# Kernel tuning notes

Measured on AMD Instinct MI355X. Metric: run time of the kernel, lower is better.

Reference implementation:

```python
import jax, jax.numpy as jnp
import numpy as np

B, T, F = 512, 256, 64
H = [128, 256, 128, 64]

def _glorot(key, shape):
    fan_in, fan_out = shape[0], shape[1]
    lim = np.sqrt(6.0 / (fan_in + fan_out))
    return jax.random.uniform(key, shape, jnp.float32, -lim, lim)

def setup_inputs() -> dict:
    key = jax.random.key(0)
    ks = jax.random.split(key, 16)
    inp = {"x": jax.random.normal(ks[0], (B, T, F), jnp.float32)}
    dims = [F] + H
    for i in range(4):
        inp[f"Wx{i+1}"] = _glorot(ks[1 + 3 * i], (dims[i], dims[i + 1]))
        # keras uses orthogonal recurrent init; scaled normal is an acceptable stand-in
        q, _ = jnp.linalg.qr(jax.random.normal(ks[2 + 3 * i], (dims[i + 1], dims[i + 1])))
        inp[f"Wh{i+1}"] = q.astype(jnp.float32)
        inp[f"b{i+1}"] = jnp.zeros((dims[i + 1],), jnp.float32)
    inp["Wd"] = _glorot(ks[13], (T * H[-1], 1))
    inp["bd"] = jnp.zeros((1,), jnp.float32)
    return inp

def simple_rnn(x, Wx, Wh, b):
    # x: [B, T, Fin] -> hidden sequence [B, T, H]; h_t = relu(x_t Wx + h_{t-1} Wh + b)
    xp = jnp.einsum('btf,fh->tbh', x, Wx) + b  # precompute input projection, time-major
    h0 = jnp.zeros((x.shape[0], Wh.shape[0]), x.dtype)
    def step(h, xt):
        h = jax.nn.relu(xt + h @ Wh)
        return h, h
    _, hs = jax.lax.scan(step, h0, xp)  # hs: [T, B, H]
    return jnp.transpose(hs, (1, 0, 2))

def reference(x, Wx1, Wh1, b1, Wx2, Wh2, b2, Wx3, Wh3, b3, Wx4, Wh4, b4, Wd, bd):
    h = simple_rnn(x, Wx1, Wh1, b1)   # dropout layers are identity at inference
    h = simple_rnn(h, Wx2, Wh2, b2)
    h = simple_rnn(h, Wx3, Wh3, b3)
    h = simple_rnn(h, Wx4, Wh4, b4)
    flat = h.reshape(h.shape[0], -1)  # [B, T*64]
    return flat @ Wd + bd             # [B, 1]
```

## Files before the change

kernel.cpp:

```cpp
#include <hip/hip_runtime.h>
#include <hip/hip_bf16.h>

#define BB 512
#define TT 256

typedef __attribute__((ext_vector_type(8))) short bf16x8;
typedef __attribute__((ext_vector_type(4))) float f32x4;

__device__ __forceinline__ unsigned short f2b(float f) {
    union { float f; unsigned u; } v; v.f = f;
    unsigned r = v.u + 0x7FFFu + ((v.u >> 16) & 1u);
    return (unsigned short)(r >> 16);
}
__device__ __forceinline__ float b2f(unsigned short h) {
    union { unsigned u; float f; } v; v.u = ((unsigned)h) << 16;
    return v.f;
}
__device__ __forceinline__ ushort2 pk2(float a, float b) {
    __hip_bfloat162 h = __float22bfloat162_rn(float2{a, b});
    union { __hip_bfloat162 h; ushort2 u; } v; v.h = h; return v.u;
}


__global__ __launch_bounds__(256) void cvt_tile4(const float* __restrict__ x,
                                                 unsigned short* __restrict__ xb,
                                                 const float* __restrict__ bd,
                                                 float* __restrict__ out) {
    if (blockIdx.x == 0) {
        out[threadIdx.x] = bd[0];
        out[threadIdx.x + 256] = bd[0];
    }
    const int s = blockIdx.x >> 6;
    const int tg = blockIdx.x & 63;
    const int wv = threadIdx.x >> 6;
    const int lane = threadIdx.x & 63;
    const int t = tg * 4 + wv;
    const int f0 = (lane & 15) * 4;
    const float* xt = x + ((size_t)s * 16 * TT + t) * 64;
    unsigned short* ob = xb + ((size_t)s * TT + t) * 1024;
#pragma unroll
    for (int it = 0; it < 4; ++it) {
        const int b = it * 4 + (lane >> 4);
        float4 v = *reinterpret_cast<const float4*>(xt + (size_t)b * (TT * 64) + f0);
        ushort2 lo = pk2(v.x, v.y), hi = pk2(v.z, v.w);
        ushort4 o; o.x = lo.x; o.y = lo.y; o.z = hi.x; o.w = hi.y;
        *reinterpret_cast<ushort4*>(ob + (f0 >> 3) * 128 + b * 8 + (f0 & 7)) = o;
    }
}

__global__ __launch_bounds__(512) __attribute__((amdgpu_waves_per_eu(2, 2))) void rnn4(
    const unsigned short* __restrict__ Xb,
    const float* __restrict__ Wx1, const float* __restrict__ Wh1, const float* __restrict__ b1,
    const float* __restrict__ Wx2, const float* __restrict__ Wh2, const float* __restrict__ b2,
    const float* __restrict__ Wx3, const float* __restrict__ Wh3, const float* __restrict__ b3,
    const float* __restrict__ Wx4, const float* __restrict__ Wh4, const float* __restrict__ b4,
    unsigned short* __restrict__ H4) {
    const int tid = threadIdx.x;
    const int s = blockIdx.x;
    const int w = tid >> 6;
    const int lane = tid & 63;
    const int l15 = lane & 15;
    const int quad = lane >> 4;
    const int rdo = quad * 128 + l15 * 8;

    __shared__ __align__(16) unsigned short hall[2][9216];

    bf16x8 wreg[48];
    f32x4 bvv[6];

#define LOADW(BASE, WP, H_, CB, KC_, MT_)                                          \
    _Pragma("unroll")                                                              \
    for (int mt = 0; mt < MT_; ++mt) {                                             \
        int m = (CB) + mt * 16 + l15;                                              \
        _Pragma("unroll")                                                          \
        for (int kc = 0; kc < KC_; ++kc)                                           \
            _Pragma("unroll")                                                      \
            for (int j = 0; j < 8; ++j)                                            \
                wreg[(BASE) + kc * MT_ + mt][j] =                                  \
                    (short)f2b(WP[(kc * 32 + quad * 8 + j) * H_ + m]);             \
    }
#define LOADBF(OFF, BP, CB, MT_)                                                   \
    _Pragma("unroll")                                                              \
    for (int mt = 0; mt < MT_; ++mt) {                                             \
        float4 t4v = *reinterpret_cast<const float4*>((BP) + (CB) + mt * 16 + quad * 4); \
        bvv[(OFF) + mt][0] = t4v.x; bvv[(OFF) + mt][1] = t4v.y;                    \
        bvv[(OFF) + mt][2] = t4v.z; bvv[(OFF) + mt][3] = t4v.w;                    \
    }

    if (w < 2) {
        LOADW(0,  Wh1, 128, w * 64, 4, 4)
        LOADW(16, Wx1, 128, w * 64, 2, 4)
        LOADW(24, Wh4, 64,  w * 32, 2, 2)
        LOADW(28, Wx4, 64,  w * 32, 4, 2)
        LOADBF(0, b1, w * 64, 4)
        LOADBF(4, b4, w * 32, 2)
    } else if (w < 6) {
        __builtin_amdgcn_s_setprio(1);
        LOADW(0,  Wh2, 256, (w - 2) * 64, 8, 4)
        LOADW(32, Wx2, 256, (w - 2) * 64, 4, 4)
        LOADBF(0, b2, (w - 2) * 64, 4)
    } else {
        LOADW(0,  Wh3, 128, (w - 6) * 64, 4, 4)
        LOADW(16, Wx3, 128, (w - 6) * 64, 8, 4)
        LOADBF(0, b3, (w - 6) * 64, 4)
    }
#undef LOADW
#undef LOADBF

    for (int i = tid; i < 2 * 9216; i += 512) (&hall[0][0])[i] = 0;

    const unsigned short* Xs = Xb + (size_t)s * TT * 1024;
    unsigned short* H4s = H4 + (size_t)s * TT * 1024;

    if (w < 2) {
#pragma unroll
        for (int kx = 0; kx < 2; ++kx) {
            wreg[36 + kx] = *reinterpret_cast<const bf16x8*>(&Xs[kx * 512 + rdo]);
            wreg[38 + kx] = *reinterpret_cast<const bf16x8*>(&Xs[1024 + kx * 512 + rdo]);
        }
    }
    __syncthreads();

    const unsigned short* xp0 = Xs + 2 * 1024 + rdo;
    const unsigned short* xp1 = Xs + 3 * 1024 + rdo;

    const int wro1 = (w * 8 + (quad >> 1)) * 128 + l15 * 8 + (quad & 1) * 4;
    const int wro4 = 8192 + (w * 4 + (quad >> 1)) * 128 + l15 * 8 + (quad & 1) * 4;
    const int wro2 = 2048 + ((w - 2) * 8 + (quad >> 1)) * 128 + l15 * 8 + (quad & 1) * 4;
    const int wro3 = 6144 + ((w - 6) * 8 + (quad >> 1)) * 128 + l15 * 8 + (quad & 1) * 4;

    unsigned short* op_e = H4s + 1024 + (wro4 - 8192);
    unsigned short* op_o = H4s + (wro4 - 8192);

#define PACKMK(ACC_MT)                                                             \
    ushort2 lo = pk2(fmaxf((ACC_MT)[0], 0.f), fmaxf((ACC_MT)[1], 0.f));            \
    ushort2 hi = pk2(fmaxf((ACC_MT)[2], 0.f), fmaxf((ACC_MT)[3], 0.f));            \
    ushort4 o; o.x = lo.x; o.y = lo.y; o.z = hi.x; o.w = hi.y;

#define STEP(TAU_, RP_, WP_, XAB, XPP, OPP)                                        \
    {                                                                              \
        const int tau_ = (TAU_);                                                   \
        const unsigned short* RB = &hall[RP_][0];                                  \
        unsigned short* WB = &hall[WP_][0];                                        \
        if (w < 2) {                                                               \
            if ((unsigned)tau_ < TT) {                                     \
                f32x4 acc[4];                                                      \
                _Pragma("unroll")                                                  \
                for (int mt = 0; mt < 4; ++mt)                                     \
                    acc[mt] = __builtin_amdgcn_mfma_f32_16x16x32_bf16(             \
                        wreg[16 + mt], wreg[(XAB) + 0], bvv[mt], 0, 0, 0);         \
                _Pragma("unroll")                                                  \
                for (int mt = 0; mt < 4; ++mt)                                     \
                    acc[mt] = __builtin_amdgcn_mfma_f32_16x16x32_bf16(             \
                        wreg[20 + mt], wreg[(XAB) + 1], acc[mt], 0, 0, 0);         \
                if (tau_ + 2 < TT) {                                               \
                    wreg[(XAB) + 0] = *reinterpret_cast<const bf16x8*>(XPP);       \
                    wreg[(XAB) + 1] = *reinterpret_cast<const bf16x8*>(XPP + 512); \
                    XPP += 2048;                                                   \
                }                                                                  \
                _Pragma("unroll")                                                  \
                for (int kc = 0; kc < 4; ++kc) {                                   \
                    bf16x8 af = *reinterpret_cast<const bf16x8*>(&RB[rdo + kc * 512]); \
                    _Pragma("unroll")                                              \
                    for (int mt = 0; mt < 4; ++mt)                                 \
                        acc[mt] = __builtin_amdgcn_mfma_f32_16x16x32_bf16(         \
                            wreg[kc * 4 + mt], af, acc[mt], 0, 0, 0);              \
                }                                                                  \
                _Pragma("unroll")                                                  \
                for (int mt = 0; mt < 4; ++mt) {                                   \
                    PACKMK(acc[mt])                                                \
                    *reinterpret_cast<ushort4*>(&WB[wro1 + mt * 256]) = o;         \
                }                                                                  \
            }                                                                      \
            if ((unsigned)(tau_ - 3) < TT) {                               \
                f32x4 acc[2];                                                      \
                {                                                                  \
                    bf16x8 af0 = *reinterpret_cast<const bf16x8*>(&RB[6144 + rdo]); \
                    _Pragma("unroll")                                              \
                    for (int mt = 0; mt < 2; ++mt)                                 \
                        acc[mt] = __builtin_amdgcn_mfma_f32_16x16x32_bf16(         \
                            wreg[28 + mt], af0, bvv[4 + mt], 0, 0, 0);             \
                }                                                                  \
                _Pragma("unroll")                                                  \
                for (int kx = 1; kx < 4; ++kx) {                                   \
                    bf16x8 af = *reinterpret_cast<const bf16x8*>(&RB[6144 + rdo + kx * 512]); \
                    _Pragma("unroll")                                              \
                    for (int mt = 0; mt < 2; ++mt)                                 \
                        acc[mt] = __builtin_amdgcn_mfma_f32_16x16x32_bf16(         \
                            wreg[28 + kx * 2 + mt], af, acc[mt], 0, 0, 0);         \
                }                                                                  \
                _Pragma("unroll")                                                  \
                for (int kc = 0; kc < 2; ++kc) {                                   \
                    bf16x8 af = *reinterpret_cast<const bf16x8*>(&RB[8192 + rdo + kc * 512]); \
                    _Pragma("unroll")                                              \
                    for (int mt = 0; mt < 2; ++mt)                                 \
                        acc[mt] = __builtin_amdgcn_mfma_f32_16x16x32_bf16(         \
                            wreg[24 + kc * 2 + mt], af, acc[mt], 0, 0, 0);         \
                }                                                                  \
                _Pragma("unroll")                                                  \
                for (int mt = 0; mt < 2; ++mt) {                                   \
                    PACKMK(acc[mt])                                                \
                    *reinterpret_cast<ushort4*>(&WB[wro4 + mt * 256]) = o;         \
                    *reinterpret_cast<ushort4*>(OPP + mt * 256) = o;               \
                }                                                                  \
                OPP += 2048;                                                       \
            }                                                                      \
        } else if (w < 6) {                                                        \
            if ((unsigned)(tau_ - 1) < TT) {                               \
                f32x4 acc[4];                                                      \
                {                                                                  \
                    bf16x8 af0 = *reinterpret_cast<const bf16x8*>(&RB[rdo]);       \
                    _Pragma("unroll")                                              \
                    for (int mt = 0; mt < 4; ++mt)                                 \
                        acc[mt] = __builtin_amdgcn_mfma_f32_16x16x32_bf16(         \
                            wreg[32 + mt], af0, bvv[mt], 0, 0, 0);                 \
                }                                                                  \
                _Pragma("unroll")                                                  \
                for (int kx = 1; kx < 4; ++kx) {                                   \
                    bf16x8 af = *reinterpret_cast<const bf16x8*>(&RB[rdo + kx * 512]); \
                    _Pragma("unroll")                                              \
                    for (int mt = 0; mt < 4; ++mt)                                 \
                        acc[mt] = __builtin_amdgcn_mfma_f32_16x16x32_bf16(         \
                            wreg[32 + kx * 4 + mt], af, acc[mt], 0, 0, 0);         \
                }                                                                  \
                _Pragma("unroll")                                                  \
                for (int kc = 0; kc < 8; ++kc) {                                   \
                    bf16x8 af = *reinterpret_cast<const bf16x8*>(&RB[2048 + rdo + kc * 512]); \
                    _Pragma("unroll")                                              \
                    for (int mt = 0; mt < 4; ++mt)                                 \
                        acc[mt] = __builtin_amdgcn_mfma_f32_16x16x32_bf16(         \
                            wreg[kc * 4 + mt], af, acc[mt], 0, 0, 0);              \
                }                                                                  \
                _Pragma("unroll")                                                  \
                for (int mt = 0; mt < 4; ++mt) {                                   \
                    PACKMK(acc[mt])                                                \
                    *reinterpret_cast<ushort4*>(&WB[wro2 + mt * 256]) = o;         \
                }                                                                  \
            }                                                                      \
        } else {                                                                   \
            if ((unsigned)(tau_ - 2) < TT) {                               \
                f32x4 acc[4];                                                      \
                {                                                                  \
                    bf16x8 af0 = *reinterpret_cast<const bf16x8*>(&RB[2048 + rdo]); \
                    _Pragma("unroll")                                              \
                    for (int mt = 0; mt < 4; ++mt)                                 \
                        acc[mt] = __builtin_amdgcn_mfma_f32_16x16x32_bf16(         \
                            wreg[16 + mt], af0, bvv[mt], 0, 0, 0);                 \
                }                                                                  \
                _Pragma("unroll")                                                  \
                for (int kx = 1; kx < 8; ++kx) {                                   \
                    bf16x8 af = *reinterpret_cast<const bf16x8*>(&RB[2048 + rdo + kx * 512]); \
                    _Pragma("unroll")                                              \
                    for (int mt = 0; mt < 4; ++mt)                                 \
                        acc[mt] = __builtin_amdgcn_mfma_f32_16x16x32_bf16(         \
                            wreg[16 + kx * 4 + mt], af, acc[mt], 0, 0, 0);         \
                }                                                                  \
                _Pragma("unroll")                                                  \
                for (int kc = 0; kc < 4; ++kc) {                                   \
                    bf16x8 af = *reinterpret_cast<const bf16x8*>(&RB[6144 + rdo + kc * 512]); \
                    _Pragma("unroll")                                              \
                    for (int mt = 0; mt < 4; ++mt)                                 \
                        acc[mt] = __builtin_amdgcn_mfma_f32_16x16x32_bf16(         \
                            wreg[kc * 4 + mt], af, acc[mt], 0, 0, 0);              \
                }                                                                  \
                _Pragma("unroll")                                                  \
                for (int mt = 0; mt < 4; ++mt) {                                   \
                    PACKMK(acc[mt])                                                \
                    *reinterpret_cast<ushort4*>(&WB[wro3 + mt * 256]) = o;         \
                }                                                                  \
            }                                                                      \
        }                                                                          \
        __builtin_amdgcn_s_waitcnt(0xC07F);                                        \
        __builtin_amdgcn_s_barrier();                                              \
    }

#pragma unroll 1
    for (int tau = 0; tau < TT + 3; tau += 2) {
        STEP(tau, 0, 1, 36, xp0, op_e)
        STEP(tau + 1, 1, 0, 38, xp1, op_o)
    }
#undef STEP
#undef PACKMK
}

__global__ __launch_bounds__(256) void dense_part(const unsigned short* __restrict__ Ht,
                                                  const float* __restrict__ Wd,
                                                  float* __restrict__ out) {
    __shared__ float red[16][17];
    const int s = blockIdx.x >> 3;
    const int tc = blockIdx.x & 7;
    const int tid = threadIdx.x;
    const int b = (tid >> 1) & 15;
    const int kbase = (tid >> 5) * 8 + (tid & 1) * 4;
    const unsigned short* base = Ht + ((size_t)s * TT + tc * 32) * 1024 + tid * 4;
    float acc = 0.f;
    for (int t = 0; t < 32; ++t) {
        ushort4 v = *reinterpret_cast<const ushort4*>(base + (size_t)t * 1024);
        const float* wd = &Wd[(tc * 32 + t) * 64 + kbase];
        acc += b2f(v.x) * wd[0] + b2f(v.y) * wd[1] + b2f(v.z) * wd[2] + b2f(v.w) * wd[3];
    }
    red[b][(tid >> 5) * 2 + (tid & 1)] = acc;
    __syncthreads();
    if (tid < 16) {
        float sum = 0.f;
#pragma unroll
        for (int j = 0; j < 16; ++j) sum += red[tid][j];
        atomicAdd(&out[s * 16 + tid], sum);
    }
}

extern "C" void kernel_launch(void* const* d_in, const int* in_sizes, int n_in,
                              void* d_out, int out_size, void* d_ws, size_t ws_size,
                              hipStream_t stream) {
    (void)in_sizes; (void)n_in; (void)out_size; (void)ws_size;
    const float* x   = (const float*)d_in[0];
    const float* Wx1 = (const float*)d_in[1];
    const float* Wh1 = (const float*)d_in[2];
    const float* b1  = (const float*)d_in[3];
    const float* Wx2 = (const float*)d_in[4];
    const float* Wh2 = (const float*)d_in[5];
    const float* b2  = (const float*)d_in[6];
    const float* Wx3 = (const float*)d_in[7];
    const float* Wh3 = (const float*)d_in[8];
    const float* b3  = (const float*)d_in[9];
    const float* Wx4 = (const float*)d_in[10];
    const float* Wh4 = (const float*)d_in[11];
    const float* b4  = (const float*)d_in[12];
    const float* Wd  = (const float*)d_in[13];
    const float* bd  = (const float*)d_in[14];
    float* out = (float*)d_out;

    char* ws = (char*)d_ws;
    unsigned short* xbT = (unsigned short*)(ws);
    unsigned short* H4  = (unsigned short*)(ws + 16777216);

    cvt_tile4<<<2048, 256, 0, stream>>>(x, xbT, bd, out);

    rnn4<<<32, 512, 0, stream>>>(xbT, Wx1, Wh1, b1, Wx2, Wh2, b2,
                                 Wx3, Wh3, b3, Wx4, Wh4, b4, H4);

    dense_part<<<256, 256, 0, stream>>>(H4, Wd, out);
}
```

Before: 421.7 us.

## Fuse dense head into RNN kernel and stage cvt transpose through LDS

The final dense projection moves into the tail of the recurrent kernel. Each block reads back its own H4 slice after a waitcnt and barrier, reduces it in LDS, adds the bias and writes the output directly. This removes a kernel launch and the atomics along with the separate out-initialisation. The input conversion kernel now loads rows with coalesced float4 reads into shared memory and writes 8-wide bf16 packs, where before it used strided per-lane accesses. Risks: the fused tail relies on H4s (not visible) and on global writes from the same block being visible after the barrier, and the dense work runs on only 32 blocks.

```diff
diff --git a/kernel.cpp b/kernel.cpp
--- a/kernel.cpp
+++ b/kernel.cpp
@@ -23,28 +23,35 @@
 
 
 __global__ __launch_bounds__(256) void cvt_tile4(const float* __restrict__ x,
-                                                 unsigned short* __restrict__ xb,
-                                                 const float* __restrict__ bd,
-                                                 float* __restrict__ out) {
-    if (blockIdx.x == 0) {
-        out[threadIdx.x] = bd[0];
-        out[threadIdx.x + 256] = bd[0];
-    }
+                                                 unsigned short* __restrict__ xb) {
+    __shared__ float xs[16][260];
     const int s = blockIdx.x >> 6;
     const int tg = blockIdx.x & 63;
-    const int wv = threadIdx.x >> 6;
-    const int lane = threadIdx.x & 63;
-    const int t = tg * 4 + wv;
-    const int f0 = (lane & 15) * 4;
-    const float* xt = x + ((size_t)s * 16 * TT + t) * 64;
-    unsigned short* ob = xb + ((size_t)s * TT + t) * 1024;
+    const int tid = threadIdx.x;
+    const float* xbase = x + ((size_t)(s * 16) * TT + tg * 4) * 64;
 #pragma unroll
     for (int it = 0; it < 4; ++it) {
-        const int b = it * 4 + (lane >> 4);
-        float4 v = *reinterpret_cast<const float4*>(xt + (size_t)b * (TT * 64) + f0);
-        ushort2 lo = pk2(v.x, v.y), hi = pk2(v.z, v.w);
-        ushort4 o; o.x = lo.x; o.y = lo.y; o.z = hi.x; o.w = hi.y;
-        *reinterpret_cast<ushort4*>(ob + (f0 >> 3) * 128 + b * 8 + (f0 & 7)) = o;
+        const int b = it * 4 + (tid >> 6);
+        const int r = tid & 63;
+        float4 v = *reinterpret_cast<const float4*>(xbase + (size_t)b * (TT * 64) + r * 4);
+        *reinterpret_cast<float4*>(&xs[b][r * 4]) = v;
+    }
+    __syncthreads();
+#pragma unroll
+    for (int it = 0; it < 2; ++it) {
+        const int t = it * 2 + (tid >> 7);
+        const int oct = (tid >> 4) & 7;
+        const int b = tid & 15;
+        const float* src = &xs[b][t * 64 + oct * 8];
+        float4 va = *reinterpret_cast<const float4*>(src);
+        float4 vb = *reinterpret_cast<const float4*>(src + 4);
+        ushort2 p0 = pk2(va.x, va.y), p1 = pk2(va.z, va.w);
+        ushort2 p2 = pk2(vb.x, vb.y), p3 = pk2(vb.z, vb.w);
+        ushort4 lo; lo.x = p0.x; lo.y = p0.y; lo.z = p1.x; lo.w = p1.y;
+        ushort4 hi; hi.x = p2.x; hi.y = p2.y; hi.z = p3.x; hi.w = p3.y;
+        unsigned short* ob = xb + ((size_t)(s * TT) + tg * 4 + t) * 1024 + oct * 128 + b * 8;
+        *reinterpret_cast<ushort4*>(ob) = lo;
+        *reinterpret_cast<ushort4*>(ob + 4) = hi;
     }
 }
 
@@ -54,7 +61,9 @@
     const float* __restrict__ Wx2, const float* __restrict__ Wh2, const float* __restrict__ b2,
     const float* __restrict__ Wx3, const float* __restrict__ Wh3, const float* __restrict__ b3,
     const float* __restrict__ Wx4, const float* __restrict__ Wh4, const float* __restrict__ b4,
-    unsigned short* __restrict__ H4) {
+    unsigned short* __restrict__ H4,
+    const float* __restrict__ Wd, const float* __restrict__ bd,
+    float* __restrict__ out) {
     const int tid = threadIdx.x;
     const int s = blockIdx.x;
     const int w = tid >> 6;
@@ -281,31 +290,41 @@
     }
 #undef STEP
 #undef PACKMK
-}
-
-__global__ __launch_bounds__(256) void dense_part(const unsigned short* __restrict__ Ht,
-                                                  const float* __restrict__ Wd,
-                                                  float* __restrict__ out) {
-    __shared__ float red[16][17];
-    const int s = blockIdx.x >> 3;
-    const int tc = blockIdx.x & 7;
-    const int tid = threadIdx.x;
-    const int b = (tid >> 1) & 15;
-    const int kbase = (tid >> 5) * 8 + (tid & 1) * 4;
-    const unsigned short* base = Ht + ((size_t)s * TT + tc * 32) * 1024 + tid * 4;
-    float acc = 0.f;
-    for (int t = 0; t < 32; ++t) {
-        ushort4 v = *reinterpret_cast<const ushort4*>(base + (size_t)t * 1024);
-        const float* wd = &Wd[(tc * 32 + t) * 64 + kbase];
-        acc += b2f(v.x) * wd[0] + b2f(v.y) * wd[1] + b2f(v.z) * wd[2] + b2f(v.w) * wd[3];
-    }
-    red[b][(tid >> 5) * 2 + (tid & 1)] = acc;
+
+    __builtin_amdgcn_s_waitcnt(0x0F70);
     __syncthreads();
-    if (tid < 16) {
-        float sum = 0.f;
+    {
+        float dacc = 0.f;
+        const unsigned short* gb = H4s + quad * 128 + l15 * 8;
+        const float* wb = Wd + quad * 8;
+#pragma unroll 4
+        for (int ti = 0; ti < 32; ++ti) {
+            const int t = w + ti * 8;
+            bf16x8 h0 = *reinterpret_cast<const bf16x8*>(gb + (size_t)t * 1024);
+            bf16x8 h1 = *reinterpret_cast<const bf16x8*>(gb + (size_t)t * 1024 + 512);
+            const float* wd = wb + t * 64;
+            float4 wa = *reinterpret_cast<const float4*>(wd);
+            float4 wc = *reinterpret_cast<const float4*>(wd + 4);
+            float4 we = *reinterpret_cast<const float4*>(wd + 32);
+            float4 wg = *reinterpret_cast<const float4*>(wd + 36);
+            dacc += b2f((unsigned short)h0[0]) * wa.x + b2f((unsigned short)h0[1]) * wa.y +
+                    b2f((unsigned short)h0[2]) * wa.z + b2f((unsigned short)h0[3]) * wa.w +
+                    b2f((unsigned short)h0[4]) * wc.x + b2f((unsigned short)h0[5]) * wc.y +
+                    b2f((unsigned short)h0[6]) * wc.z + b2f((unsigned short)h0[7]) * wc.w +
+                    b2f((unsigned short)h1[0]) * we.x + b2f((unsigned short)h1[1]) * we.y +
+                    b2f((unsigned short)h1[2]) * we.z + b2f((unsigned short)h1[3]) * we.w +
+                    b2f((unsigned short)h1[4]) * wg.x + b2f((unsigned short)h1[5]) * wg.y +
+                    b2f((unsigned short)h1[6]) * wg.z + b2f((unsigned short)h1[7]) * wg.w;
+        }
+        float* red = reinterpret_cast<float*>(&hall[0][0]);
+        red[(w * 4 + quad) * 16 + l15] = dacc;
+        __syncthreads();
+        if (tid < 16) {
+            float sum = bd[0];
 #pragma unroll
-        for (int j = 0; j < 16; ++j) sum += red[tid][j];
-        atomicAdd(&out[s * 16 + tid], sum);
+            for (int j = 0; j < 32; ++j) sum += red[j * 16 + tid];
+            out[s * 16 + tid] = sum;
+        }
     }
 }
 
@@ -334,10 +353,8 @@
     unsigned short* xbT = (unsigned short*)(ws);
     unsigned short* H4  = (unsigned short*)(ws + 16777216);
 
-    cvt_tile4<<<2048, 256, 0, stream>>>(x, xbT, bd, out);
+    cvt_tile4<<<2048, 256, 0, stream>>>(x, xbT);
 
     rnn4<<<32, 512, 0, stream>>>(xbT, Wx1, Wh1, b1, Wx2, Wh2, b2,
-                                 Wx3, Wh3, b3, Wx4, Wh4, b4, H4);
-
-    dense_part<<<256, 256, 0, stream>>>(H4, Wd, out);
-}
+                                 Wx3, Wh3, b3, Wx4, Wh4, b4, H4, Wd, bd, out);
+}
```

Result: no change. 423.5 us (+0.4%).

## Deepen layer wavefront pipeline with triple-buffered LDS and register prefetch

Applied to the files above, without the earlier changes.

The layered RNN wavefront moves from a two-buffer LDS ping-pong to a rotating three-buffer scheme, and each layer's stage skew grows from one step to two. Each wave group now loads the previous layer's input rows into registers (pf) one step ahead and does all LDS reads before issuing its MFMA chains, so LDS latency overlaps the previous barrier interval. The input conversion kernel is also rewritten to stage x through shared memory, giving coalesced reads and 16-byte writes. The cost is a longer pipeline fill and drain (TT+6 steps instead of TT+3), more LDS use and higher register pressure.

```diff
diff --git a/kernel.cpp b/kernel.cpp
--- a/kernel.cpp
+++ b/kernel.cpp
@@ -30,21 +30,34 @@
         out[threadIdx.x] = bd[0];
         out[threadIdx.x + 256] = bd[0];
     }
+    __shared__ float xs[16][260];
     const int s = blockIdx.x >> 6;
     const int tg = blockIdx.x & 63;
-    const int wv = threadIdx.x >> 6;
-    const int lane = threadIdx.x & 63;
-    const int t = tg * 4 + wv;
-    const int f0 = (lane & 15) * 4;
-    const float* xt = x + ((size_t)s * 16 * TT + t) * 64;
-    unsigned short* ob = xb + ((size_t)s * TT + t) * 1024;
+    const int tid = threadIdx.x;
+    const float* xbase = x + ((size_t)(s * 16) * TT + tg * 4) * 64;
 #pragma unroll
     for (int it = 0; it < 4; ++it) {
-        const int b = it * 4 + (lane >> 4);
-        float4 v = *reinterpret_cast<const float4*>(xt + (size_t)b * (TT * 64) + f0);
-        ushort2 lo = pk2(v.x, v.y), hi = pk2(v.z, v.w);
-        ushort4 o; o.x = lo.x; o.y = lo.y; o.z = hi.x; o.w = hi.y;
-        *reinterpret_cast<ushort4*>(ob + (f0 >> 3) * 128 + b * 8 + (f0 & 7)) = o;
+        const int b = it * 4 + (tid >> 6);
+        const int r = tid & 63;
+        float4 v = *reinterpret_cast<const float4*>(xbase + (size_t)b * (TT * 64) + r * 4);
+        *reinterpret_cast<float4*>(&xs[b][r * 4]) = v;
+    }
+    __syncthreads();
+#pragma unroll
+    for (int it = 0; it < 2; ++it) {
+        const int t = it * 2 + (tid >> 7);
+        const int oct = (tid >> 4) & 7;
+        const int b = tid & 15;
+        const float* src = &xs[b][t * 64 + oct * 8];
+        float4 va = *reinterpret_cast<const float4*>(src);
+        float4 vb = *reinterpret_cast<const float4*>(src + 4);
+        ushort2 p0 = pk2(va.x, va.y), p1 = pk2(va.z, va.w);
+        ushort2 p2 = pk2(vb.x, vb.y), p3 = pk2(vb.z, vb.w);
+        ushort4 lo; lo.x = p0.x; lo.y = p0.y; lo.z = p1.x; lo.w = p1.y;
+        ushort4 hi; hi.x = p2.x; hi.y = p2.y; hi.z = p3.x; hi.w = p3.y;
+        unsigned short* ob = xb + ((size_t)(s * TT) + tg * 4 + t) * 1024 + oct * 128 + b * 8;
+        *reinterpret_cast<ushort4*>(ob) = lo;
+        *reinterpret_cast<ushort4*>(ob + 4) = hi;
     }
 }
 
@@ -63,9 +76,10 @@
     const int quad = lane >> 4;
     const int rdo = quad * 128 + l15 * 8;
 
-    __shared__ __align__(16) unsigned short hall[2][9216];
+    __shared__ __align__(16) unsigned short hall[3][9216];
 
     bf16x8 wreg[48];
+    bf16x8 pf[4];
     f32x4 bvv[6];
 
 #define LOADW(BASE, WP, H_, CB, KC_, MT_)                                          \
@@ -107,7 +121,7 @@
 #undef LOADW
 #undef LOADBF
 
-    for (int i = tid; i < 2 * 9216; i += 512) (&hall[0][0])[i] = 0;
+    for (int i = tid; i < 3 * 9216; i += 512) (&hall[0][0])[i] = 0;
 
     const unsigned short* Xs = Xb + (size_t)s * TT * 1024;
     unsigned short* H4s = H4 + (size_t)s * TT * 1024;
@@ -129,21 +143,26 @@
     const int wro2 = 2048 + ((w - 2) * 8 + (quad >> 1)) * 128 + l15 * 8 + (quad & 1) * 4;
     const int wro3 = 6144 + ((w - 6) * 8 + (quad >> 1)) * 128 + l15 * 8 + (quad & 1) * 4;
 
-    unsigned short* op_e = H4s + 1024 + (wro4 - 8192);
-    unsigned short* op_o = H4s + (wro4 - 8192);
+    unsigned short* op_e = H4s + (wro4 - 8192);
+    unsigned short* op_o = H4s + 1024 + (wro4 - 8192);
 
 #define PACKMK(ACC_MT)                                                             \
     ushort2 lo = pk2(fmaxf((ACC_MT)[0], 0.f), fmaxf((ACC_MT)[1], 0.f));            \
     ushort2 hi = pk2(fmaxf((ACC_MT)[2], 0.f), fmaxf((ACC_MT)[3], 0.f));            \
     ushort4 o; o.x = lo.x; o.y = lo.y; o.z = hi.x; o.w = hi.y;
 
-#define STEP(TAU_, RP_, WP_, XAB, XPP, OPP)                                        \
+#define STEP(TAU_, RBP_, WBP_, IBP_, XAB, XPP, OPP)                                \
     {                                                                              \
         const int tau_ = (TAU_);                                                   \
-        const unsigned short* RB = &hall[RP_][0];                                  \
-        unsigned short* WB = &hall[WP_][0];                                        \
+        const unsigned short* RB = (RBP_);                                         \
+        unsigned short* WB = (WBP_);                                               \
+        const unsigned short* IB = (IBP_);                                         \
         if (w < 2) {                                                               \
-            if ((unsigned)tau_ < TT) {                                     \
+            if ((unsigned)tau_ < TT) {                            \
+                bf16x8 rf[4];                                                      \
+                _Pragma("unroll")                                                  \
+                for (int kc = 0; kc < 4; ++kc)                                     \
+                    rf[kc] = *reinterpret_cast<const bf16x8*>(&RB[rdo + kc * 512]); \
                 f32x4 acc[4];                                                      \
                 _Pragma("unroll")                                                  \
                 for (int mt = 0; mt < 4; ++mt)                                     \
@@ -159,44 +178,39 @@
                     XPP += 2048;                                                   \
                 }                                                                  \
                 _Pragma("unroll")                                                  \
-                for (int kc = 0; kc < 4; ++kc) {                                   \
-                    bf16x8 af = *reinterpret_cast<const bf16x8*>(&RB[rdo + kc * 512]); \
-                    _Pragma("unroll")                                              \
-                    for (int mt = 0; mt < 4; ++mt)                                 \
-                        acc[mt] = __builtin_amdgcn_mfma_f32_16x16x32_bf16(         \
-                            wreg[kc * 4 + mt], af, acc[mt], 0, 0, 0);              \
-                }                                                                  \
+                for (int kc = 0; kc < 4; ++kc)                                     \
+                    _Pragma("unroll")                                              \
+                    for (int mt = 0; mt < 4; ++mt)                                 \
+                        acc[mt] = __builtin_amdgcn_mfma_f32_16x16x32_bf16(         \
+                            wreg[kc * 4 + mt], rf[kc], acc[mt], 0, 0, 0);          \
                 _Pragma("unroll")                                                  \
                 for (int mt = 0; mt < 4; ++mt) {                                   \
                     PACKMK(acc[mt])                                                \
                     *reinterpret_cast<ushort4*>(&WB[wro1 + mt * 256]) = o;         \
                 }                                                                  \
             }                                                                      \
-            if ((unsigned)(tau_ - 3) < TT) {                               \
+            if ((unsigned)(tau_ - 6) < TT) {  \
+                bf16x8 rf4[2];                                                     \
+                _Pragma("unroll")                                                  \
+                for (int kc = 0; kc < 2; ++kc)                                     \
+                    rf4[kc] = *reinterpret_cast<const bf16x8*>(&RB[8192 + rdo + kc * 512]); \
                 f32x4 acc[2];                                                      \
-                {                                                                  \
-                    bf16x8 af0 = *reinterpret_cast<const bf16x8*>(&RB[6144 + rdo]); \
+                _Pragma("unroll")                                                  \
+                for (int mt = 0; mt < 2; ++mt)                                     \
+                    acc[mt] = __builtin_amdgcn_mfma_f32_16x16x32_bf16(             \
+                        wreg[28 + mt], pf[0], bvv[4 + mt], 0, 0, 0);               \
+                _Pragma("unroll")                                                  \
+                for (int kx = 1; kx < 4; ++kx)                                     \
                     _Pragma("unroll")                                              \
                     for (int mt = 0; mt < 2; ++mt)                                 \
                         acc[mt] = __builtin_amdgcn_mfma_f32_16x16x32_bf16(         \
-                            wreg[28 + mt], af0, bvv[4 + mt], 0, 0, 0);             \
-                }                                                                  \
-                _Pragma("unroll")                                                  \
-                for (int kx = 1; kx < 4; ++kx) {                                   \
-                    bf16x8 af = *reinterpret_cast<const bf16x8*>(&RB[6144 + rdo + kx * 512]); \
+                            wreg[28 + kx * 2 + mt], pf[kx], acc[mt], 0, 0, 0);     \
+                _Pragma("unroll")                                                  \
+                for (int kc = 0; kc < 2; ++kc)                                     \
                     _Pragma("unroll")                                              \
                     for (int mt = 0; mt < 2; ++mt)                                 \
                         acc[mt] = __builtin_amdgcn_mfma_f32_16x16x32_bf16(         \
-                            wreg[28 + kx * 2 + mt], af, acc[mt], 0, 0, 0);         \
-                }                                                                  \
-                _Pragma("unroll")                                                  \
-                for (int kc = 0; kc < 2; ++kc) {                                   \
-                    bf16x8 af = *reinterpret_cast<const bf16x8*>(&RB[8192 + rdo + kc * 512]); \
-                    _Pragma("unroll")                                              \
-                    for (int mt = 0; mt < 2; ++mt)                                 \
-                        acc[mt] = __builtin_amdgcn_mfma_f32_16x16x32_bf16(         \
-                            wreg[24 + kc * 2 + mt], af, acc[mt], 0, 0, 0);         \
-                }                                                                  \
+                            wreg[24 + kc * 2 + mt], rf4[kc], acc[mt], 0, 0, 0);    \
                 _Pragma("unroll")                                                  \
                 for (int mt = 0; mt < 2; ++mt) {                                   \
                     PACKMK(acc[mt])                                                \
@@ -205,79 +219,104 @@
                 }                                                                  \
                 OPP += 2048;                                                       \
             }                                                                      \
+            if ((unsigned)(tau_ - 5) < TT) {   \
+                _Pragma("unroll")                                                  \
+                for (int kx = 0; kx < 4; ++kx)                                     \
+                    pf[kx] = *reinterpret_cast<const bf16x8*>(&RB[6144 + rdo + kx * 512]); \
+            }                                                                      \
         } else if (w < 6) {                                                        \
-            if ((unsigned)(tau_ - 1) < TT) {                               \
+            if ((unsigned)(tau_ - 2) < TT) {  \
+                bf16x8 rf[8];                                                      \
+                _Pragma("unroll")                                                  \
+                for (int kc = 0; kc < 8; ++kc)                                     \
+                    rf[kc] = *reinterpret_cast<const bf16x8*>(&RB[2048 + rdo + kc * 512]); \
                 f32x4 acc[4];                                                      \
-                {                                                                  \
-                    bf16x8 af0 = *reinterpret_cast<const bf16x8*>(&RB[rdo]);       \
-                    _Pragma("unroll")                                              \
-                    for (int mt = 0; mt < 4; ++mt)                                 \
-                        acc[mt] = __builtin_amdgcn_mfma_f32_16x16x32_bf16(         \
-                            wreg[32 + mt], af0, bvv[mt], 0, 0, 0);                 \
-                }                                                                  \
-                _Pragma("unroll")                                                  \
-                for (int kx = 1; kx < 4; ++kx) {                                   \
-                    bf16x8 af = *reinterpret_cast<const bf16x8*>(&RB[rdo + kx * 512]); \
-                    _Pragma("unroll")                                              \
-                    for (int mt = 0; mt < 4; ++mt)                                 \
-                        acc[mt] = __builtin_amdgcn_mfma_f32_16x16x32_bf16(         \
-                            wreg[32 + kx * 4 + mt], af, acc[mt], 0, 0, 0);         \
-                }                                                                  \
-                _Pragma("unroll")                                                  \
-                for (int kc = 0; kc < 8; ++kc) {                                   \
-                    bf16x8 af = *reinterpret_cast<const bf16x8*>(&RB[2048 + rdo + kc * 512]); \
-                    _Pragma("unroll")                                              \
-                    for (int mt = 0; mt < 4; ++mt)                                 \
-                        acc[mt] = __builtin_amdgcn_mfma_f32_16x16x32_bf16(         \
-                            wreg[kc * 4 + mt], af, acc[mt], 0, 0, 0);              \
-                }                                                                  \
+                _Pragma("unroll")                                                  \
+                for (int mt = 0; mt < 4; ++mt)                                     \
+                    acc[mt] = __builtin_amdgcn_mfma_f32_16x16x32_bf16(             \
+                        wreg[32 + mt], pf[0], bvv[mt], 0, 0, 0);                   \
+                _Pragma("unroll")                                                  \
+                for (int kx = 1; kx < 4; ++kx)                                     \
+                    _Pragma("unroll")                                              \
+                    for (int mt = 0; mt < 4; ++mt)                                 \
+                        acc[mt] = __builtin_amdgcn_mfma_f32_16x16x32_bf16(         \
+                            wreg[32 + kx * 4 + mt], pf[kx], acc[mt], 0, 0, 0);     \
+                _Pragma("unroll")                                                  \
+                for (int kc = 0; kc < 8; ++kc)                                     \
+                    _Pragma("unroll")                                              \
+                    for (int mt = 0; mt < 4; ++mt)                                 \
+                        acc[mt] = __builtin_amdgcn_mfma_f32_16x16x32_bf16(         \
+                            wreg[kc * 4 + mt], rf[kc], acc[mt], 0, 0, 0);          \
                 _Pragma("unroll")                                                  \
                 for (int mt = 0; mt < 4; ++mt) {                                   \
                     PACKMK(acc[mt])                                                \
                     *reinterpret_cast<ushort4*>(&WB[wro2 + mt * 256]) = o;         \
                 }                                                                  \
             }                                                                      \
+            if ((unsigned)(tau_ - 1) < TT) {   \
+                _Pragma("unroll")                                                  \
+                for (int kx = 0; kx < 4; ++kx)                                     \
+                    pf[kx] = *reinterpret_cast<const bf16x8*>(&RB[rdo + kx * 512]); \
+            }                                                                      \
         } else {                                                                   \
-            if ((unsigned)(tau_ - 2) < TT) {                               \
+            if ((unsigned)(tau_ - 4) < TT) {                    \
+                bf16x8 rf2[4];          \
+                _Pragma("unroll")                                                  \
+                for (int kx = 0; kx < 4; ++kx)                                     \
+                    rf2[kx] = *reinterpret_cast<const bf16x8*>(&IB[2048 + rdo + (4 + kx) * 512]); \
+                bf16x8 rf[4];               \
+                _Pragma("unroll")                                                  \
+                for (int kc = 0; kc < 4; ++kc)                                     \
+                    rf[kc] = *reinterpret_cast<const bf16x8*>(&RB[6144 + rdo + kc * 512]); \
                 f32x4 acc[4];                                                      \
-                {                                                                  \
-                    bf16x8 af0 = *reinterpret_cast<const bf16x8*>(&RB[2048 + rdo]); \
-                    _Pragma("unroll")                                              \
-                    for (int mt = 0; mt < 4; ++mt)                                 \
-                        acc[mt] = __builtin_amdgcn_mfma_f32_16x16x32_bf16(         \
-                            wreg[16 + mt], af0, bvv[mt], 0, 0, 0);                 \
-                }                                                                  \
-                _Pragma("unroll")                                                  \
-                for (int kx = 1; kx < 8; ++kx) {                                   \
-                    bf16x8 af = *reinterpret_cast<const bf16x8*>(&RB[2048 + rdo + kx * 512]); \
-                    _Pragma("unroll")                                              \
-                    for (int mt = 0; mt < 4; ++mt)                                 \
-                        acc[mt] = __builtin_amdgcn_mfma_f32_16x16x32_bf16(         \
-                            wreg[16 + kx * 4 + mt], af, acc[mt], 0, 0, 0);         \
-                }                                                                  \
-                _Pragma("unroll")                                                  \
-                for (int kc = 0; kc < 4; ++kc) {                                   \
-                    bf16x8 af = *reinterpret_cast<const bf16x8*>(&RB[6144 + rdo + kc * 512]); \
-                    _Pragma("unroll")                                              \
-                    for (int mt = 0; mt < 4; ++mt)                                 \
-                        acc[mt] = __builtin_amdgcn_mfma_f32_16x16x32_bf16(         \
-                            wreg[kc * 4 + mt], af, acc[mt], 0, 0, 0);              \
-                }                                                                  \
+                _Pragma("unroll")                                                  \
+                for (int mt = 0; mt < 4; ++mt)                                     \
+                    acc[mt] = __builtin_amdgcn_mfma_f32_16x16x32_bf16(             \
+                        wreg[16 + mt], pf[0], bvv[mt], 0, 0, 0);                   \
+                _Pragma("unroll")                                                  \
+                for (int kx = 1; kx < 4; ++kx)                                     \
+                    _Pragma("unroll")                                              \
+                    for (int mt = 0; mt < 4; ++mt)                                 \
+                        acc[mt] = __builtin_amdgcn_mfma_f32_16x16x32_bf16(         \
+                            wreg[16 + kx * 4 + mt], pf[kx], acc[mt], 0, 0, 0);     \
+                _Pragma("unroll")                                                  \
+                for (int kx = 0; kx < 4; ++kx)                                     \
+                    _Pragma("unroll")                                              \
+                    for (int mt = 0; mt < 4; ++mt)                                 \
+                        acc[mt] = __builtin_amdgcn_mfma_f32_16x16x32_bf16(         \
+                            wreg[32 + kx * 4 + mt], rf2[kx], acc[mt], 0, 0, 0);    \
+                _Pragma("unroll")                                                  \
+                for (int kc = 0; kc < 4; ++kc)                                     \
+                    _Pragma("unroll")                                              \
+                    for (int mt = 0; mt < 4; ++mt)                                 \
+                        acc[mt] = __builtin_amdgcn_mfma_f32_16x16x32_bf16(         \
+                            wreg[kc * 4 + mt], rf[kc], acc[mt], 0, 0, 0);          \
                 _Pragma("unroll")                                                  \
                 for (int mt = 0; mt < 4; ++mt) {                                   \
                     PACKMK(acc[mt])                                                \
                     *reinterpret_cast<ushort4*>(&WB[wro3 + mt * 256]) = o;         \
                 }                                                                  \
             }                                                                      \
+            if ((unsigned)(tau_ - 3) < TT) {    \
+                _Pragma("unroll")                                                  \
+                for (int kx = 0; kx < 4; ++kx)                                     \
+                    pf[kx] = *reinterpret_cast<const bf16x8*>(&RB[2048 + rdo + kx * 512]); \
+            }                                                                      \
         }                                                                          \
         __builtin_amdgcn_s_waitcnt(0xC07F);                                        \
         __builtin_amdgcn_s_barrier();                                              \
     }
 
+    unsigned short* bprv = &hall[2][0];
+    unsigned short* bcur = &hall[0][0];
+    unsigned short* bnxt = &hall[1][0];
+
 #pragma unroll 1
-    for (int tau = 0; tau < TT + 3; tau += 2) {
-        STEP(tau, 0, 1, 36, xp0, op_e)
-        STEP(tau + 1, 1, 0, 38, xp1, op_o)
+    for (int tau = 0; tau < TT + 6; tau += 2) {
+        STEP(tau, bprv, bcur, bnxt, 36, xp0, op_e)
+        { unsigned short* t_ = bprv; bprv = bcur; bcur = bnxt; bnxt = t_; }
+        STEP(tau + 1, bprv, bcur, bnxt, 38, xp1, op_o)
+        { unsigned short* t_ = bprv; bprv = bcur; bcur = bnxt; bnxt = t_; }
     }
 #undef STEP
 #undef PACKMK
```

Result: slower. 681.6 us (+61.6%).
